# Kernel optimization log

Measured on AMD Instinct MI355X. Metric: run time of the kernel, lower is better.

Reference implementation:

```python
import jax, jax.numpy as jnp
import numpy as np

GATE_THRESHOLD = 0.5
GATE_TEMPERATURE = 1.0

B, T, H, R = 4, 4096, 2048, 512


def setup_inputs() -> dict:
    key = jax.random.key(0)
    k1, k2, k3 = jax.random.split(key, 3)
    x = jax.random.normal(k1, (B, T, H), dtype=jnp.float32)
    mask = jax.random.randint(k2, (B, T), 0, 2).astype(bool)
    W_A = jax.random.normal(k3, (R, H), dtype=jnp.float32) * 0.02  # nn.Linear weight [out, in]
    gate_scale = jnp.ones((1,), dtype=jnp.float32)
    gate_bias = jnp.full((1,), -1e-6, dtype=jnp.float32)
    return {"x": x, "mask": mask, "W_A": W_A, "gate_scale": gate_scale, "gate_bias": gate_bias}


def reference(x, mask, W_A, gate_scale, gate_bias):
    # Torch code gathers valid tokens, projects, norms, scales/biases, thresholds,
    # then scatters mask/score back. In jax (static shapes) we compute on all
    # tokens with invalid rows zeroed; outputs match the scattered torch outputs.
    orig_lead = x.shape[:-1]                       # (B, T)
    x_flat = x.reshape(-1, x.shape[-1])            # [N, H]
    mask_flat = mask.reshape(-1)                   # [N] bool
    x_valid = jnp.where(mask_flat[:, None], x_flat, 0.0)
    gate_hidden = jnp.einsum('nh,rh->nr', x_valid, W_A)        # [N, R]
    gate_score = jnp.sqrt(jnp.sum(gate_hidden * gate_hidden, axis=-1))  # L2 norm, [N]
    gate_score = gate_score * gate_scale[0] - gate_bias[0]
    thr = GATE_THRESHOLD / GATE_TEMPERATURE
    gate_mask_full = mask_flat & (gate_score >= thr)
    gate_score_full = jnp.where(gate_mask_full, gate_score, -jnp.inf)
    return (gate_mask_full.reshape(orig_lead),
            gate_score_full.reshape(orig_lead),
            gate_hidden)
```

## Files before the change

kernel.cpp:

```cpp
#include <hip/hip_runtime.h>
#include <hip/hip_bf16.h>
#include <math.h>

#define H_DIM 2048
#define R_DIM 512
#define NTOK  16384
#define BM    64
#define BN    128
#define BK    64
#define KST   (H_DIM / BK)
#define NEG_BIG (-1.0e30f)

typedef __attribute__((ext_vector_type(8))) short bf16x8;
typedef __attribute__((ext_vector_type(4))) float f32x4;

static __device__ __forceinline__ unsigned short f2bf(float f) {
    __hip_bfloat16 h = __float2bfloat16(f);
    return *reinterpret_cast<unsigned short*>(&h);
}

static __device__ __forceinline__ bf16x8 pack8(float4 lo, float4 hi) {
    union { bf16x8 v; unsigned short u[8]; } t;
    t.u[0] = f2bf(lo.x); t.u[1] = f2bf(lo.y); t.u[2] = f2bf(lo.z); t.u[3] = f2bf(lo.w);
    t.u[4] = f2bf(hi.x); t.u[5] = f2bf(hi.y); t.u[6] = f2bf(hi.z); t.u[7] = f2bf(hi.w);
    return t.v;
}

static __device__ __forceinline__ void gll16(const void* g, void* l) {
    __builtin_amdgcn_global_load_lds(
        (const __attribute__((address_space(1))) unsigned int*)g,
        (__attribute__((address_space(3))) unsigned int*)l,
        16, 0, 0);
}

__global__ __launch_bounds__(1024) void rfg15_aux(
    const float* __restrict__ W, unsigned short* __restrict__ Wb,
    const unsigned char* __restrict__ msk,
    int* __restrict__ vidx, int* __restrict__ nv_out)
{
    __shared__ int Wt[16];
    __shared__ int Wbase[16];
    const int b   = blockIdx.x;
    const int tid = threadIdx.x;

    if (b < 128) {
        const int i  = b * 1024 + tid;
        const int r  = i >> 8;
        const int k8 = i & 255;
        const float* src = W + (size_t)r * H_DIM + k8 * 8;
        float4 a = *reinterpret_cast<const float4*>(src);
        float4 c = *reinterpret_cast<const float4*>(src + 4);
        *reinterpret_cast<bf16x8*>(Wb + ((size_t)k8 * R_DIM + r) * 8) = pack8(a, c);
    } else {
        const int lane = tid & 63;
        const int wv   = tid >> 6;
        union { uint4 v; unsigned char c[16]; } u;
        u.v = *reinterpret_cast<const uint4*>(msk + tid * 16);
        const unsigned int s4 = u.v.x + u.v.y + u.v.z + u.v.w;
        const int cnt = (s4 & 0xFF) + ((s4 >> 8) & 0xFF)
                      + ((s4 >> 16) & 0xFF) + (s4 >> 24);
        int pfx = cnt;
        #pragma unroll
        for (int off = 1; off < 64; off <<= 1) {
            const int t = __shfl_up(pfx, off, 64);
            if (lane >= off) pfx += t;
        }
        if (lane == 63) Wt[wv] = pfx;
        __syncthreads();
        if (tid == 0) {
            int run = 0;
            for (int i = 0; i < 16; ++i) { Wbase[i] = run; run += Wt[i]; }
        }
        __syncthreads();
        int p = Wbase[wv] + pfx - cnt;
        #pragma unroll
        for (int j = 0; j < 16; ++j)
            if (u.c[j]) vidx[p++] = tid * 16 + j;
        if (tid == 1023) {
            const int total = Wbase[15] + Wt[15];
            nv_out[0] = total;
            const int pe = (total + 63) & ~63;
            for (int i = total; i < pe; ++i) vidx[i] = 0;
        }
    }
}

__global__ __launch_bounds__(256, 2) void rfg15_gemm(
    const float* __restrict__ x,
    const unsigned char* __restrict__ msk,
    const unsigned short* __restrict__ Wb,
    const int* __restrict__ vidx,
    const int* __restrict__ nvp,
    float* __restrict__ part,
    float* __restrict__ hid)
{
    __shared__ __align__(16) float4 As[2][1024];
    __shared__ __align__(16) short  Bs[2][1024][8];
    __shared__ float Ps[2][BM];
    __shared__ int   Vr[BM];
    __shared__ int   Vv[BM];

    const int nv  = nvp[0];
    const int tid = threadIdx.x;
    const int bid   = blockIdx.x;
    const int xcd   = bid & 7;
    const int local = bid >> 3;
    const int nt    = local & 3;
    const int mt    = (local >> 2) * 8 + xcd;
    const int m0    = mt * BM;

    if (m0 >= nv) {
        const int mt_min = (nv + 63) >> 6;
        const int Z = (256 - mt_min) * 4;
        const int z = (mt - mt_min) * 4 + nt;
        const float2 z2 = make_float2(0.f, 0.f);
        for (int t = z; t < NTOK; t += Z)
            if (!msk[t])
                *reinterpret_cast<float2*>(&hid[(size_t)t * R_DIM + tid * 2]) = z2;
        return;
    }
    const int n0 = nt * BN;

    const int w  = tid >> 6;
    const int l  = tid & 63;
    const int wr = w >> 1;
    const int wc = w & 1;
    const int fr = l & 15;
    const int fg = l >> 4;

    int vrj[4];
    #pragma unroll
    for (int j = 0; j < 4; ++j)
        vrj[j] = vidx[m0 + (tid >> 4) + 16 * j];
    if (tid < BM) {
        Vr[tid] = vidx[m0 + tid];
        Vv[tid] = (m0 + tid) < nv;
    }

    f32x4 acc[2][4] = {};

#define RFG15_STAGE(ks_, buf_) do {                                      \
        const int _kA = (ks_) * BK;                                      \
        _Pragma("unroll")                                                \
        for (int j = 0; j < 4; ++j) {                                    \
            const int idx = j * 256 + tid;                               \
            const int row = idx >> 4, cL = idx & 15;                     \
            const int cG  = cL ^ (row & 7);                              \
            gll16(x + (size_t)vrj[j] * H_DIM + _kA + cG * 4,             \
                  (char*)&As[buf_][0] + idx * 16);                       \
        }                                                                \
        _Pragma("unroll")                                                \
        for (int j = 0; j < 4; ++j) {                                    \
            const int idx = j * 256 + tid;                               \
            const int k8 = idx >> 7, col = idx & 127;                    \
            gll16(Wb + ((size_t)((ks_) * 8 + k8) * R_DIM + n0 + col) * 8,\
                  (char*)&Bs[buf_][0][0] + idx * 16);                    \
        }                                                                \
    } while (0)

#define RFG15_BODY(ks_, buf_, stage_)  do {                              \
        bf16x8 bfr[2][4];                                                \
        _Pragma("unroll")                                                \
        for (int kk = 0; kk < 2; ++kk)                                   \
            _Pragma("unroll")                                            \
            for (int ni = 0; ni < 4; ++ni)                               \
                bfr[kk][ni] = *reinterpret_cast<const bf16x8*>(          \
                    &Bs[buf_][(kk * 4 + fg) * 128 + wc * 64 + ni * 16 + fr][0]); \
        bf16x8 afr[2][2];                                                \
        _Pragma("unroll")                                                \
        for (int mi = 0; mi < 2; ++mi) {                                 \
            const int row = wr * 32 + mi * 16 + fr;                      \
            const int s   = row & 7;                                     \
            _Pragma("unroll")                                            \
            for (int kk = 0; kk < 2; ++kk) {                             \
                const int g0 = kk * 8 + 2 * fg;                          \
                float4 lo = As[buf_][row * 16 + (g0 ^ s)];               \
                float4 hi = As[buf_][row * 16 + ((g0 + 1) ^ s)];         \
                afr[mi][kk] = pack8(lo, hi);                             \
            }                                                            \
        }                                                                \
        asm volatile("s_waitcnt lgkmcnt(0)" ::: "memory");               \
        __builtin_amdgcn_s_barrier();       \
        if (stage_) RFG15_STAGE((ks_) + 2, buf_);                        \
        __builtin_amdgcn_s_setprio(1);                                   \
        _Pragma("unroll")                                                \
        for (int kk = 0; kk < 2; ++kk)                                   \
            _Pragma("unroll")                                            \
            for (int mi = 0; mi < 2; ++mi)                               \
                _Pragma("unroll")                                        \
                for (int ni = 0; ni < 4; ++ni)                           \
                    acc[mi][ni] = __builtin_amdgcn_mfma_f32_16x16x32_bf16(\
                        afr[mi][kk], bfr[kk][ni], acc[mi][ni], 0, 0, 0); \
        __builtin_amdgcn_s_setprio(0);                                   \
    } while (0)

    RFG15_STAGE(0, 0);
    RFG15_STAGE(1, 1);

    for (int ks = 0; ks < KST - 2; ++ks) {
        asm volatile("s_waitcnt vmcnt(8)" ::: "memory");
        __builtin_amdgcn_s_barrier();
        RFG15_BODY(ks, (ks & 1), true);
    }
    {
        asm volatile("s_waitcnt vmcnt(8)" ::: "memory");
        __builtin_amdgcn_s_barrier();
        RFG15_BODY(KST - 2, ((KST - 2) & 1), false);
    }
    {
        asm volatile("s_waitcnt vmcnt(0)" ::: "memory");
        __builtin_amdgcn_s_barrier();
        RFG15_BODY(KST - 1, ((KST - 1) & 1), false);
    }
#undef RFG15_BODY
#undef RFG15_STAGE

    #pragma unroll
    for (int mi = 0; mi < 2; ++mi) {
        #pragma unroll
        for (int r = 0; r < 4; ++r) {
            const int rowl = wr * 32 + mi * 16 + fg * 4 + r;
            float s = 0.0f;
            #pragma unroll
            for (int ni = 0; ni < 4; ++ni) {
                const float v = acc[mi][ni][r];
                s = fmaf(v, v, s);
            }
            #pragma unroll
            for (int off = 1; off < 16; off <<= 1)
                s += __shfl_xor(s, off, 64);
            if (fr == 0) Ps[wc][rowl] = s;
        }
    }

    #pragma unroll
    for (int mi = 0; mi < 2; ++mi)
        #pragma unroll
        for (int ni = 0; ni < 4; ++ni)
            #pragma unroll
            for (int r = 0; r < 4; ++r) {
                const int rowl = wr * 32 + mi * 16 + fg * 4 + r;
                if (Vv[rowl])
                    hid[(size_t)Vr[rowl] * R_DIM + n0 + wc * 64 + ni * 16 + fr] =
                        acc[mi][ni][r];
            }

    __syncthreads();
    if (tid < BM && Vv[tid])
        part[(size_t)nt * NTOK + Vr[tid]] = Ps[0][tid] + Ps[1][tid];
}

__global__ __launch_bounds__(256) void rfg15_score(
    const unsigned char* __restrict__ msk,
    const float* __restrict__ gsc,
    const float* __restrict__ gbi,
    const float* __restrict__ part,
    float* __restrict__ om,
    float* __restrict__ os)
{
    const int t = blockIdx.x * 256 + threadIdx.x;
    const float s = part[t] + part[NTOK + t] + part[2 * NTOK + t] + part[3 * NTOK + t];
    float sc = sqrtf(s) * gsc[0] - gbi[0];
    if (!(sc > -1.0e30f && sc < 1.0e30f)) sc = 0.0f;
    const bool keep = (msk[t] != 0) && (sc >= 0.5f);
    om[t] = keep ? 1.0f : 0.0f;
    os[t] = keep ? sc : NEG_BIG;
}

extern "C" void kernel_launch(void* const* d_in, const int* in_sizes, int n_in,
                              void* d_out, int out_size, void* d_ws, size_t ws_size,
                              hipStream_t stream)
{
    const float*         x     = (const float*)d_in[0];
    const unsigned char* msk   = (const unsigned char*)d_in[1];
    const float*         W     = (const float*)d_in[2];
    const float*         scale = (const float*)d_in[3];
    const float*         bias  = (const float*)d_in[4];

    float* out = (float*)d_out;
    float* om  = out;
    float* os  = out + NTOK;
    float* hid = out + 2 * NTOK;

    char* ws = (char*)d_ws;
    unsigned short* Wb   = (unsigned short*)ws;
    float*          part = (float*)(ws + 2 * 1024 * 1024);
    int*            vidx = (int*)(ws + 2 * 1024 * 1024 + 256 * 1024);
    int*            nvp  = (int*)(ws + 2 * 1024 * 1024 + 320 * 1024);

    rfg15_aux<<<129, 1024, 0, stream>>>(W, Wb, msk, vidx, nvp);
    rfg15_gemm<<<(NTOK / BM) * (R_DIM / BN), 256, 0, stream>>>(
        x, msk, Wb, vidx, nvp, part, hid);
    rfg15_score<<<NTOK / 256, 256, 0, stream>>>(msk, scale, bias, part, om, os);
}
```

Measured before the change: 40.35 us.

## Load A tile directly from global into registers, bypassing LDS staging

Activation rows are no longer staged in shared memory with global_load_lds. Each lane now loads its own fp32 fragments straight into registers, double-buffered one k-step ahead, and packs them to bf16 for the MFMA. Only the W tile still goes through LDS. This removes the A-side LDS traffic and the swizzled LDS reads. In exchange it uses more registers, adds per-lane strided global loads that the four wave pairs sharing rows duplicate, and changes the vmcnt waits.

```diff
diff --git a/kernel.cpp b/kernel.cpp
--- a/kernel.cpp
+++ b/kernel.cpp
@@ -33,7 +33,7 @@
         16, 0, 0);
 }
 
-__global__ __launch_bounds__(1024) void rfg15_aux(
+__global__ __launch_bounds__(1024) void rfg16_aux(
     const float* __restrict__ W, unsigned short* __restrict__ Wb,
     const unsigned char* __restrict__ msk,
     int* __restrict__ vidx, int* __restrict__ nv_out)
@@ -85,7 +85,7 @@
     }
 }
 
-__global__ __launch_bounds__(256, 2) void rfg15_gemm(
+__global__ __launch_bounds__(256, 2) void rfg16_gemm(
     const float* __restrict__ x,
     const unsigned char* __restrict__ msk,
     const unsigned short* __restrict__ Wb,
@@ -94,8 +94,7 @@
     float* __restrict__ part,
     float* __restrict__ hid)
 {
-    __shared__ __align__(16) float4 As[2][1024];
-    __shared__ __align__(16) short  Bs[2][1024][8];
+    __shared__ __align__(16) short Bs[2][1024][8];
     __shared__ float Ps[2][BM];
     __shared__ int   Vr[BM];
     __shared__ int   Vv[BM];
@@ -128,27 +127,18 @@
     const int fr = l & 15;
     const int fg = l >> 4;
 
-    int vrj[4];
-    #pragma unroll
-    for (int j = 0; j < 4; ++j)
-        vrj[j] = vidx[m0 + (tid >> 4) + 16 * j];
+    const float* pA[2];
+    pA[0] = x + (size_t)vidx[m0 + wr * 32 + fr]      * H_DIM + fg * 8;
+    pA[1] = x + (size_t)vidx[m0 + wr * 32 + 16 + fr] * H_DIM + fg * 8;
     if (tid < BM) {
         Vr[tid] = vidx[m0 + tid];
         Vv[tid] = (m0 + tid) < nv;
     }
 
     f32x4 acc[2][4] = {};
-
-#define RFG15_STAGE(ks_, buf_) do {                                      \
-        const int _kA = (ks_) * BK;                                      \
-        _Pragma("unroll")                                                \
-        for (int j = 0; j < 4; ++j) {                                    \
-            const int idx = j * 256 + tid;                               \
-            const int row = idx >> 4, cL = idx & 15;                     \
-            const int cG  = cL ^ (row & 7);                              \
-            gll16(x + (size_t)vrj[j] * H_DIM + _kA + cG * 4,             \
-                  (char*)&As[buf_][0] + idx * 16);                       \
-        }                                                                \
+    float4 Aa[2][2][2], Ab[2][2][2];
+
+#define RFG16_STAGEB(ks_, buf_) do {                                     \
         _Pragma("unroll")                                                \
         for (int j = 0; j < 4; ++j) {                                    \
             const int idx = j * 256 + tid;                               \
@@ -158,7 +148,21 @@
         }                                                                \
     } while (0)
 
-#define RFG15_BODY(ks_, buf_, stage_)  do {                              \
+#define RFG16_LOADA(ks_, D) do {                                         \
+        _Pragma("unroll")                                                \
+        for (int mi = 0; mi < 2; ++mi)                                   \
+            _Pragma("unroll")                                            \
+            for (int kk = 0; kk < 2; ++kk) {                             \
+                const float* _p = pA[mi] + (ks_) * BK + kk * 32;         \
+                D[mi][kk][0] = *reinterpret_cast<const float4*>(_p);     \
+                D[mi][kk][1] = *reinterpret_cast<const float4*>(_p + 4); \
+            }                                                            \
+    } while (0)
+
+#define RFG16_STEP(ks_, buf_, Duse, Dload, loadA_, stage_, VM) do {      \
+        asm volatile("s_waitcnt vmcnt(" VM ")" ::: "memory");            \
+        __builtin_amdgcn_s_barrier();                                    \
+        if (loadA_) RFG16_LOADA((ks_) + 1, Dload);                       \
         bf16x8 bfr[2][4];                                                \
         _Pragma("unroll")                                                \
         for (int kk = 0; kk < 2; ++kk)                                   \
@@ -166,22 +170,15 @@
             for (int ni = 0; ni < 4; ++ni)                               \
                 bfr[kk][ni] = *reinterpret_cast<const bf16x8*>(          \
                     &Bs[buf_][(kk * 4 + fg) * 128 + wc * 64 + ni * 16 + fr][0]); \
+        asm volatile("s_waitcnt lgkmcnt(0)" ::: "memory");               \
+        __builtin_amdgcn_s_barrier();      \
+        if (stage_) RFG16_STAGEB((ks_) + 2, buf_);                       \
         bf16x8 afr[2][2];                                                \
         _Pragma("unroll")                                                \
-        for (int mi = 0; mi < 2; ++mi) {                                 \
-            const int row = wr * 32 + mi * 16 + fr;                      \
-            const int s   = row & 7;                                     \
-            _Pragma("unroll")                                            \
-            for (int kk = 0; kk < 2; ++kk) {                             \
-                const int g0 = kk * 8 + 2 * fg;                          \
-                float4 lo = As[buf_][row * 16 + (g0 ^ s)];               \
-                float4 hi = As[buf_][row * 16 + ((g0 + 1) ^ s)];         \
-                afr[mi][kk] = pack8(lo, hi);                             \
-            }                                                            \
-        }                                                                \
-        asm volatile("s_waitcnt lgkmcnt(0)" ::: "memory");               \
-        __builtin_amdgcn_s_barrier();       \
-        if (stage_) RFG15_STAGE((ks_) + 2, buf_);                        \
+        for (int mi = 0; mi < 2; ++mi)                                   \
+            _Pragma("unroll")                                            \
+            for (int kk = 0; kk < 2; ++kk)                               \
+                afr[mi][kk] = pack8(Duse[mi][kk][0], Duse[mi][kk][1]);   \
         __builtin_amdgcn_s_setprio(1);                                   \
         _Pragma("unroll")                                                \
         for (int kk = 0; kk < 2; ++kk)                                   \
@@ -194,26 +191,20 @@
         __builtin_amdgcn_s_setprio(0);                                   \
     } while (0)
 
-    RFG15_STAGE(0, 0);
-    RFG15_STAGE(1, 1);
-
-    for (int ks = 0; ks < KST - 2; ++ks) {
-        asm volatile("s_waitcnt vmcnt(8)" ::: "memory");
-        __builtin_amdgcn_s_barrier();
-        RFG15_BODY(ks, (ks & 1), true);
-    }
-    {
-        asm volatile("s_waitcnt vmcnt(8)" ::: "memory");
-        __builtin_amdgcn_s_barrier();
-        RFG15_BODY(KST - 2, ((KST - 2) & 1), false);
-    }
-    {
-        asm volatile("s_waitcnt vmcnt(0)" ::: "memory");
-        __builtin_amdgcn_s_barrier();
-        RFG15_BODY(KST - 1, ((KST - 1) & 1), false);
-    }
-#undef RFG15_BODY
-#undef RFG15_STAGE
+    RFG16_STAGEB(0, 0);
+    RFG16_LOADA(0, Aa);
+    RFG16_STAGEB(1, 1);
+
+    for (int kb = 0; kb < KST - 2; kb += 2) {
+        RFG16_STEP(kb,     0, Aa, Ab, true, true, "12");
+        RFG16_STEP(kb + 1, 1, Ab, Aa, true, true, "12");
+    }
+    RFG16_STEP(KST - 2, 0, Aa, Ab, true,  false, "12");
+    RFG16_STEP(KST - 1, 1, Ab, Aa, false, false, "0");
+
+#undef RFG16_STEP
+#undef RFG16_LOADA
+#undef RFG16_STAGEB
 
     #pragma unroll
     for (int mi = 0; mi < 2; ++mi) {
@@ -250,7 +241,7 @@
         part[(size_t)nt * NTOK + Vr[tid]] = Ps[0][tid] + Ps[1][tid];
 }
 
-__global__ __launch_bounds__(256) void rfg15_score(
+__global__ __launch_bounds__(256) void rfg16_score(
     const unsigned char* __restrict__ msk,
     const float* __restrict__ gsc,
     const float* __restrict__ gbi,
@@ -288,8 +279,8 @@
     int*            vidx = (int*)(ws + 2 * 1024 * 1024 + 256 * 1024);
     int*            nvp  = (int*)(ws + 2 * 1024 * 1024 + 320 * 1024);
 
-    rfg15_aux<<<129, 1024, 0, stream>>>(W, Wb, msk, vidx, nvp);
-    rfg15_gemm<<<(NTOK / BM) * (R_DIM / BN), 256, 0, stream>>>(
+    rfg16_aux<<<129, 1024, 0, stream>>>(W, Wb, msk, vidx, nvp);
+    rfg16_gemm<<<(NTOK / BM) * (R_DIM / BN), 256, 0, stream>>>(
         x, msk, Wb, vidx, nvp, part, hid);
-    rfg15_score<<<NTOK / 256, 256, 0, stream>>>(msk, scale, bias, part, om, os);
-}
+    rfg16_score<<<NTOK / 256, 256, 0, stream>>>(msk, scale, bias, part, om, os);
+}
```

Result: slower. 64.07 us (+58.8%).
